# Kernel tuning notes

Hardware: AMD Instinct MI355X
Metric: run time of the kernel (lower is better)

Reference implementation:

```python
import jax, jax.numpy as jnp
import numpy as np

DIM, D_STATE, D_CONV, EXPAND = 1024, 16, 4, 2
D_INNER = EXPAND * DIM
DT_RANK = (DIM + 15) // 16  # 64
B, L = 2, 1024


def setup_inputs() -> dict:
    key = jax.random.key(0)
    ks = jax.random.split(key, 12)
    s = lambda k, shp, sc: jax.random.normal(k, shp, jnp.float32) * sc
    return {
        "x": s(ks[0], (B, L, DIM), 1.0),
        "ln_g": jnp.ones((DIM,), jnp.float32),
        "ln_b": jnp.zeros((DIM,), jnp.float32),
        "W_in": s(ks[1], (DIM, 2 * D_INNER), DIM ** -0.5),
        "conv_w": s(ks[2], (D_INNER, D_CONV), D_CONV ** -0.5),
        "conv_b": jnp.zeros((D_INNER,), jnp.float32),
        "W_x": s(ks[3], (D_INNER, DT_RANK + 2 * D_STATE), D_INNER ** -0.5),
        "W_dt": s(ks[4], (DT_RANK, D_INNER), DT_RANK ** -0.5),
        "b_dt": s(ks[5], (D_INNER,), 0.1),
        "A_log": jnp.log(jnp.broadcast_to(jnp.arange(1, D_STATE + 1, dtype=jnp.float32), (D_INNER, D_STATE))),
        "D_skip": jnp.ones((D_INNER,), jnp.float32),
        "W_out": s(ks[6], (D_INNER, DIM), D_INNER ** -0.5),
    }


def _mamba_block(x, ln_g, ln_b, W_in, conv_w, conv_b, W_x, W_dt, b_dt, A_log, D_skip, W_out):
    # LayerNorm over feature dim
    mu = jnp.mean(x, -1, keepdims=True)
    var = jnp.mean(jnp.square(x - mu), -1, keepdims=True)
    xn = (x - mu) * jax.lax.rsqrt(var + 1e-5) * ln_g + ln_b

    # in_proj -> (u, z), each (B, L, E)
    u, z = jnp.split(xn @ W_in, 2, axis=-1)

    # causal depthwise conv1d over L (kernel D_CONV) + SiLU
    up = jnp.pad(u, ((0, 0), (D_CONV - 1, 0), (0, 0)))
    uc = conv_b
    for k in range(D_CONV):
        uc = uc + conv_w[:, k] * up[:, k:k + L, :]
    uc = jax.nn.silu(uc)

    # input-dependent dt, B, C
    dbl = uc @ W_x
    dt = jax.nn.softplus(dbl[..., :DT_RANK] @ W_dt + b_dt)      # (B,L,E)
    Bc = dbl[..., DT_RANK:DT_RANK + D_STATE]                    # (B,L,N)
    Cc = dbl[..., DT_RANK + D_STATE:]                           # (B,L,N)

    A = -jnp.exp(A_log)                                         # (E,N)
    dA = jnp.exp(dt[..., None] * A)                             # (B,L,E,N)
    dBu = (dt * uc)[..., None] * Bc[:, :, None, :]              # (B,L,E,N)

    # selective scan: h_t = dA_t * h_{t-1} + dBu_t  (associative)
    def comb(c1, c2):
        a1, b1 = c1
        a2, b2 = c2
        return a2 * a1, a2 * b1 + b2

    _, h = jax.lax.associative_scan(comb, (dA, dBu), axis=1)

    y = jnp.einsum('blen,bln->ble', h, Cc) + uc * D_skip
    y = y * jax.nn.silu(z)
    return y @ W_out                                            # (B,L,DIM)


def reference(x, ln_g, ln_b, W_in, conv_w, conv_b, W_x, W_dt, b_dt, A_log, D_skip, W_out):
    return _mamba_block(x, ln_g, ln_b, W_in, conv_w, conv_b, W_x, W_dt, b_dt, A_log, D_skip, W_out)
```

## Files before the change

kernel.cpp:

```cpp
#include <hip/hip_runtime.h>
#include <hip/hip_bf16.h>

typedef __attribute__((ext_vector_type(4))) float  f32x4;
typedef __attribute__((ext_vector_type(8))) __bf16 bf16x8;
typedef __attribute__((ext_vector_type(8))) unsigned short u16x8;

typedef __attribute__((address_space(1))) void gvoid_t;
typedef __attribute__((address_space(3))) void lvoid_t;

__device__ __forceinline__ void gld16(const void* g, void* l) {
    __builtin_amdgcn_global_load_lds((const gvoid_t*)g, (lvoid_t*)l, 16, 0, 0);
}

template <int N> __device__ __forceinline__ void vwait() {
    if constexpr (N == 0)      asm volatile("s_waitcnt vmcnt(0)" ::: "memory");
    else if constexpr (N == 6) asm volatile("s_waitcnt vmcnt(6)" ::: "memory");
    else if constexpr (N == 8) asm volatile("s_waitcnt vmcnt(8)" ::: "memory");
}

__device__ __forceinline__ unsigned short f2bf(float f) {
    unsigned u = __builtin_bit_cast(unsigned, f);
    u += 0x7fffu + ((u >> 16) & 1u);
    return (unsigned short)(u >> 16);
}
__device__ __forceinline__ float bf2f(unsigned short u) {
    return __builtin_bit_cast(float, (unsigned)u << 16);
}
__device__ __forceinline__ float silu(float x) {
    return x / (1.f + __expf(-x));
}

__device__ __forceinline__ void powers16(float p, float* dA) {
    float p2 = p * p, p4 = p2 * p2, p8 = p4 * p4, p16 = p8 * p8;
    float q[5] = {p, p2, p4, p8, p16};
    #pragma unroll
    for (int n = 0; n < 16; ++n) {
        int m = n + 1;
        float r = 1.f;
        bool first = true;
        #pragma unroll
        for (int bit = 0; bit < 5; ++bit) {
            if (m & (1 << bit)) {
                r = first ? q[bit] : r * q[bit];
                first = false;
            }
        }
        dA[n] = r;
    }
}

__device__ __forceinline__ void tr_cvt(const float* __restrict__ in,
                                       unsigned short* __restrict__ out,
                                       int K, int N, int Npad, int bnb, int bkb,
                                       float* sh) {
    float (*t)[33] = (float(*)[33])sh;
    int bn = bnb * 32, bk = bkb * 32;
    int c = threadIdx.x & 31, r0 = threadIdx.x >> 5;
    #pragma unroll
    for (int rr = r0; rr < 32; rr += 8) {
        int k = bk + rr, n = bn + c;
        t[rr][c] = (k < K && n < N) ? in[(size_t)k * N + n] : 0.f;
    }
    __syncthreads();
    #pragma unroll
    for (int rr = r0; rr < 32; rr += 8) {
        int n = bn + rr, k = bk + c;
        if (n < Npad && k < K) out[(size_t)n * K + k] = f2bf(t[c][rr]);
    }
}

__global__ __launch_bounds__(256) void k_prep(const float* __restrict__ x,
                                              const float* __restrict__ g,
                                              const float* __restrict__ b,
                                              unsigned short* __restrict__ xn,
                                              const float* __restrict__ W_in,  unsigned short* __restrict__ WIN_T,
                                              const float* __restrict__ W_out, unsigned short* __restrict__ WOUT_T,
                                              const float* __restrict__ W_dt,  unsigned short* __restrict__ WDT_T,
                                              const float* __restrict__ W_x,   unsigned short* __restrict__ WX_T) {
    __shared__ float sh[32 * 33];
    int bid = blockIdx.x;
    if (bid < 2048) {
        int row = bid;
        const float4* xr = (const float4*)(x + (size_t)row * 1024);
        float4 v = xr[threadIdx.x];
        float s  = v.x + v.y + v.z + v.w;
        float ss = v.x*v.x + v.y*v.y + v.z*v.z + v.w*v.w;
        #pragma unroll
        for (int o = 32; o > 0; o >>= 1) { s += __shfl_down(s, o); ss += __shfl_down(ss, o); }
        if ((threadIdx.x & 63) == 0) { sh[threadIdx.x >> 6] = s; sh[4 + (threadIdx.x >> 6)] = ss; }
        __syncthreads();
        s  = sh[0] + sh[1] + sh[2] + sh[3];
        ss = sh[4] + sh[5] + sh[6] + sh[7];
        float mu  = s * (1.f / 1024.f);
        float inv = rsqrtf(ss * (1.f / 1024.f) - mu * mu + 1e-5f);
        float4 gv = ((const float4*)g)[threadIdx.x];
        float4 bv = ((const float4*)b)[threadIdx.x];
        ushort4 o4;
        o4.x = f2bf((v.x - mu) * inv * gv.x + bv.x);
        o4.y = f2bf((v.y - mu) * inv * gv.y + bv.y);
        o4.z = f2bf((v.z - mu) * inv * gv.z + bv.z);
        o4.w = f2bf((v.w - mu) * inv * gv.w + bv.w);
        ((ushort4*)xn)[(size_t)row * 256 + threadIdx.x] = o4;
    } else if (bid < 6144) {
        int i = bid - 2048;  tr_cvt(W_in,  WIN_T,  1024, 4096, 4096, i & 127, i >> 7, sh);
    } else if (bid < 8192) {
        int i = bid - 6144;  tr_cvt(W_out, WOUT_T, 2048, 1024, 1024, i & 31,  i >> 5, sh);
    } else if (bid < 8320) {
        int i = bid - 8192;  tr_cvt(W_dt,  WDT_T,  64,   2048, 2048, i & 63,  i >> 6, sh);
    } else {
        int i = bid - 8320;  tr_cvt(W_x,   WX_T,   2048, 96,   128,  i & 3,   i >> 2, sh);
    }
}

template <int BM, int BN, int EPI>
__global__ __launch_bounds__(256) void k_gemm2(const unsigned short* __restrict__ A,
                                               const unsigned short* __restrict__ Bt,
                                               float* __restrict__ C,
                                               unsigned short* __restrict__ C2,
                                               unsigned short* __restrict__ C3,
                                               int kchunk, int lda, int ldb, int ldc,
                                               size_t zstride,
                                               const float* __restrict__ bias) {
    constexpr int PA = BM / 32, PB = BN / 32, NV = PA + PB;
    constexpr int MF = BM / 32, NF = BN / 32;
    __shared__ __attribute__((aligned(16))) unsigned short sm[2 * BM * 64 + 2 * BN * 64];
    unsigned short* smA = sm;
    unsigned short* smB = sm + 2 * BM * 64;

    int tid = threadIdx.x, wave = tid >> 6, lane = tid & 63;
    int bm = blockIdx.x * BM, bn = blockIdx.y * BN;
    int kstart = blockIdx.z * kchunk;
    int nt = kchunk >> 6;
    C += (size_t)blockIdx.z * zstride;
    int wm = (wave >> 1) * (BM / 2), wn = (wave & 1) * (BN / 2);
    int lr = lane & 15, lq = lane >> 4;
    int srow = wave * 8 + (lane >> 3);
    int scg  = lane & 7;

    f32x4 acc[MF][NF] = {};

    auto STAGE = [&](int buf, int k0) {
        unsigned short* dA = smA + buf * (BM * 64) + wave * 512;
        unsigned short* dB = smB + buf * (BN * 64) + wave * 512;
        #pragma unroll
        for (int p = 0; p < PA; ++p) {
            int row = p * 32 + srow;
            int gcol = ((scg ^ (row & 7)) << 3) + k0;
            gld16(A + (size_t)(bm + row) * lda + gcol, dA + p * 2048);
        }
        #pragma unroll
        for (int p = 0; p < PB; ++p) {
            int row = p * 32 + srow;
            int gcol = ((scg ^ (row & 7)) << 3) + k0;
            gld16(Bt + (size_t)(bn + row) * ldb + gcol, dB + p * 2048);
        }
    };

    STAGE(0, kstart);
    for (int t = 0; t < nt; ++t) {
        int cur = t & 1;
        if (t + 1 < nt) { STAGE(cur ^ 1, kstart + (t + 1) * 64); vwait<NV>(); }
        else            { vwait<0>(); }
        __builtin_amdgcn_s_barrier();
        const unsigned short* sA = smA + cur * (BM * 64);
        const unsigned short* sB = smB + cur * (BN * 64);
        #pragma unroll
        for (int ks = 0; ks < 2; ++ks) {
            int cg = (ks * 4 + lq) ^ (lr & 7);
            bf16x8 af[MF], bfv[NF];
            #pragma unroll
            for (int i = 0; i < MF; ++i)
                af[i] = *(const bf16x8*)(sA + (wm + i * 16 + lr) * 64 + (cg << 3));
            #pragma unroll
            for (int i = 0; i < NF; ++i)
                bfv[i] = *(const bf16x8*)(sB + (wn + i * 16 + lr) * 64 + (cg << 3));
            #pragma unroll
            for (int mi = 0; mi < MF; ++mi)
                #pragma unroll
                for (int ni = 0; ni < NF; ++ni)
                    acc[mi][ni] = __builtin_amdgcn_mfma_f32_16x16x32_bf16(af[mi], bfv[ni], acc[mi][ni], 0, 0, 0);
        }
        __builtin_amdgcn_s_barrier();
    }

    if (EPI == 0) {
        constexpr int PADF = BN + 4;
        float* ftile = (float*)sm;
        #pragma unroll
        for (int mi = 0; mi < MF; ++mi)
            #pragma unroll
            for (int ni = 0; ni < NF; ++ni)
                #pragma unroll
                for (int v = 0; v < 4; ++v)
                    ftile[(wm + mi * 16 + (lq << 2) + v) * PADF + wn + ni * 16 + lr] = acc[mi][ni][v];
        __syncthreads();
        #pragma unroll
        for (int q = tid; q < BM * BN / 4; q += 256) {
            int row = q / (BN / 4);
            int cc  = (q % (BN / 4)) * 4;
            float4 vv = *(const float4*)(ftile + row * PADF + cc);
            *(float4*)(C + (size_t)(bm + row) * ldc + bn + cc) = vv;
        }
    } else {
        constexpr int PADH = BN + 8;
        unsigned short* stile = sm;
        unsigned short* dst;
        int bnn;
        if (EPI == 3) { dst = C2; bnn = bn; }
        else          { dst = (bn < 2048) ? C2 : C3; bnn = bn & 2047; }
        #pragma unroll
        for (int mi = 0; mi < MF; ++mi) {
            #pragma unroll
            for (int ni = 0; ni < NF; ++ni) {
                int c = bn + wn + ni * 16 + lr;
                #pragma unroll
                for (int v = 0; v < 4; ++v) {
                    float val = acc[mi][ni][v];
                    if (EPI == 3) {
                        val += bias[c];
                        val = (val > 20.f) ? val : log1pf(__expf(val));
                    } else if (bn >= 2048) {
                        val = silu(val);
                    }
                    stile[(wm + mi * 16 + (lq << 2) + v) * PADH + wn + ni * 16 + lr] = f2bf(val);
                }
            }
        }
        __syncthreads();
        #pragma unroll
        for (int q = tid; q < BM * BN / 8; q += 256) {
            int row = q / (BN / 8);
            int cc  = (q % (BN / 8)) * 8;
            u16x8 vv = *(const u16x8*)(stile + row * PADH + cc);
            *(u16x8*)(dst + (size_t)(bm + row) * ldc + bnn + cc) = vv;
        }
    }
}

__global__ __launch_bounds__(256) void k_red8(const float* __restrict__ part,
                                              float* __restrict__ dbl,
                                              unsigned short* __restrict__ dtr) {
    int idx = blockIdx.x * 256 + threadIdx.x;
    float s = 0.f;
    #pragma unroll
    for (int z = 0; z < 8; ++z) s += part[(size_t)z * 262144 + idx];
    dbl[idx] = s;
    int r = idx >> 7, c = idx & 127;
    if (c < 64) dtr[r * 64 + c] = f2bf(s);
}

__global__ __launch_bounds__(256) void k_conv2(const unsigned short* __restrict__ UB,
                                               const float* __restrict__ cw,
                                               const float* __restrict__ cb,
                                               unsigned short* __restrict__ ucb) {
    int idx = blockIdx.x * 256 + threadIdx.x;
    int e  = idx & 2047;
    int bl = idx >> 11;
    int l  = bl & 1023;
    float acc = cb[e];
    float4 wv = *(const float4*)(cw + e * 4);
    float w4[4] = {wv.x, wv.y, wv.z, wv.w};
    #pragma unroll
    for (int k = 0; k < 4; ++k) {
        int ls = l - 3 + k;
        if (ls >= 0) acc += w4[k] * bf2f(UB[(size_t)(bl - 3 + k) * 2048 + e]);
    }
    ucb[idx] = f2bf(silu(acc));
}


__global__ __launch_bounds__(256) void k_scan_p1(const unsigned short* __restrict__ ucb,
                                                 const unsigned short* __restrict__ dtb,
                                                 const float* __restrict__ dbl,
                                                 const float* __restrict__ A_log,
                                                 float* __restrict__ aggH,
                                                 float* __restrict__ sdtb) {
    __shared__ float sB[32][16];
    int bid = blockIdx.x;
    int c = bid & 31, eblk = (bid >> 5) & 7, b = bid >> 8;
    int t = threadIdx.x;
    int e = eblk * 256 + t;
    int bl0 = b * 1024 + c * 32;
    if (t < 128) {
        int r = t >> 2, j4 = t & 3;
        *(float4*)&sB[r][j4 * 4] = *(const float4*)(dbl + (size_t)(bl0 + r) * 128 + 64 + j4 * 4);
    }
    __syncthreads();
    float Aen[16];
    #pragma unroll
    for (int n = 0; n < 16; ++n) Aen[n] = -__expf(A_log[e * 16 + n]);
    bool fastA = true;
    #pragma unroll
    for (int n = 1; n < 16; ++n)
        fastA = fastA && (fabsf(Aen[n] - (n + 1) * Aen[0]) <= 1e-3f);
    float h[16];
    #pragma unroll
    for (int n = 0; n < 16; ++n) h[n] = 0.f;
    float sdt = 0.f;
    size_t iu = (size_t)bl0 * 2048 + e;
    #pragma unroll 4
    for (int l = 0; l < 32; ++l) {
        float dtv = bf2f(dtb[iu]);
        float ucv = bf2f(ucb[iu]);
        float dtu = dtv * ucv;
        float dA[16];
        if (fastA) powers16(__expf(dtv * Aen[0]), dA);
        else {
            #pragma unroll
            for (int n = 0; n < 16; ++n) dA[n] = __expf(dtv * Aen[n]);
        }
        #pragma unroll
        for (int n = 0; n < 16; ++n)
            h[n] = fmaf(dA[n], h[n], dtu * sB[l][n]);
        sdt += dtv;
        iu += 2048;
    }
    size_t o = ((size_t)(b * 32 + c) * 16) * 2048 + e;
    #pragma unroll
    for (int n = 0; n < 16; ++n) aggH[o + (size_t)n * 2048] = h[n];
    sdtb[(size_t)(b * 32 + c) * 2048 + e] = sdt;
}

__global__ __launch_bounds__(256) void k_scan_p2(const float* __restrict__ aggH,
                                                 const float* __restrict__ sdtb,
                                                 const float* __restrict__ A_log,
                                                 float* __restrict__ hinit) {
    int idx = blockIdx.x * 256 + threadIdx.x;
    int b = idx >> 15;
    int n = (idx >> 11) & 15;
    int e = idx & 2047;
    float Aen = -__expf(A_log[e * 16 + n]);
    float h = 0.f;
    #pragma unroll 4
    for (int c = 0; c < 32; ++c) {
        size_t base = ((size_t)(b * 32 + c) * 16 + n) * 2048 + e;
        hinit[base] = h;
        float a = __expf(sdtb[(size_t)(b * 32 + c) * 2048 + e] * Aen);
        h = fmaf(a, h, aggH[base]);
    }
}

__global__ __launch_bounds__(256) void k_scan_p3(const unsigned short* __restrict__ ucb,
                                                 const unsigned short* __restrict__ dtb,
                                                 const float* __restrict__ dbl,
                                                 const unsigned short* __restrict__ sz,
                                                 const float* __restrict__ A_log,
                                                 const float* __restrict__ D_skip,
                                                 const float* __restrict__ hinit,
                                                 unsigned short* __restrict__ yg) {
    __shared__ float sBC[32][32];
    int bid = blockIdx.x;
    int c = bid & 31, eblk = (bid >> 5) & 7, b = bid >> 8;
    int t = threadIdx.x;
    int e = eblk * 256 + t;
    int bl0 = b * 1024 + c * 32;
    {
        int r = t >> 3, j = t & 7;
        *(float4*)&sBC[r][j * 4] = *(const float4*)(dbl + (size_t)(bl0 + r) * 128 + 64 + j * 4);
    }
    __syncthreads();
    float Aen[16];
    #pragma unroll
    for (int n = 0; n < 16; ++n) Aen[n] = -__expf(A_log[e * 16 + n]);
    bool fastA = true;
    #pragma unroll
    for (int n = 1; n < 16; ++n)
        fastA = fastA && (fabsf(Aen[n] - (n + 1) * Aen[0]) <= 1e-3f);
    float De = D_skip[e];
    size_t o = ((size_t)(b * 32 + c) * 16) * 2048 + e;
    float h[16];
    #pragma unroll
    for (int n = 0; n < 16; ++n) h[n] = hinit[o + (size_t)n * 2048];
    size_t iu = (size_t)bl0 * 2048 + e;
    #pragma unroll 4
    for (int l = 0; l < 32; ++l) {
        float dtv = bf2f(dtb[iu]);
        float ucv = bf2f(ucb[iu]);
        float szv = bf2f(sz[iu]);
        float dtu = dtv * ucv;
        float dA[16];
        if (fastA) powers16(__expf(dtv * Aen[0]), dA);
        else {
            #pragma unroll
            for (int n = 0; n < 16; ++n) dA[n] = __expf(dtv * Aen[n]);
        }
        float y0 = 0.f, y1 = 0.f, y2 = 0.f, y3 = 0.f;
        #pragma unroll
        for (int n = 0; n < 16; n += 4) {
            h[n]     = fmaf(dA[n],     h[n],     dtu * sBC[l][n]);
            h[n + 1] = fmaf(dA[n + 1], h[n + 1], dtu * sBC[l][n + 1]);
            h[n + 2] = fmaf(dA[n + 2], h[n + 2], dtu * sBC[l][n + 2]);
            h[n + 3] = fmaf(dA[n + 3], h[n + 3], dtu * sBC[l][n + 3]);
            y0 = fmaf(h[n],     sBC[l][16 + n],     y0);
            y1 = fmaf(h[n + 1], sBC[l][16 + n + 1], y1);
            y2 = fmaf(h[n + 2], sBC[l][16 + n + 2], y2);
            y3 = fmaf(h[n + 3], sBC[l][16 + n + 3], y3);
        }
        float y = (y0 + y1) + (y2 + y3);
        y = (y + ucv * De) * szv;
        yg[iu] = f2bf(y);
        iu += 2048;
    }
}

extern "C" void kernel_launch(void* const* d_in, const int* in_sizes, int n_in,
                              void* d_out, int out_size, void* d_ws, size_t ws_size,
                              hipStream_t stream) {
    const float* x      = (const float*)d_in[0];
    const float* ln_g   = (const float*)d_in[1];
    const float* ln_b   = (const float*)d_in[2];
    const float* W_in   = (const float*)d_in[3];
    const float* conv_w = (const float*)d_in[4];
    const float* conv_b = (const float*)d_in[5];
    const float* W_x    = (const float*)d_in[6];
    const float* W_dt   = (const float*)d_in[7];
    const float* b_dt   = (const float*)d_in[8];
    const float* A_log  = (const float*)d_in[9];
    const float* D_skip = (const float*)d_in[10];
    const float* W_out  = (const float*)d_in[11];
    float* out = (float*)d_out;

    const size_t needed =
        (size_t)4096 * 1024 * 2 + (size_t)1024 * 2048 * 2 + (size_t)2048 * 64 * 2 +
        (size_t)128 * 2048 * 2 + (size_t)2048 * 1024 * 2 + (size_t)2048 * 4096 * 4 +
        (size_t)2048 * 2048 * 4 + (size_t)2048 * 2048 * 2 + (size_t)2048 * 128 * 4 +
        (size_t)2048 * 64 * 2 + (size_t)2048 * 2048 * 4 + (size_t)2048 * 2048 * 2;
    if (ws_size < needed) return;

    char* w = (char*)d_ws;
    unsigned short* WIN_T  = (unsigned short*)w; w += (size_t)4096 * 1024 * 2;
    unsigned short* WOUT_T = (unsigned short*)w; w += (size_t)1024 * 2048 * 2;
    unsigned short* WDT_T  = (unsigned short*)w; w += (size_t)2048 * 64 * 2;
    unsigned short* WX_T   = (unsigned short*)w; w += (size_t)128 * 2048 * 2;
    unsigned short* XN     = (unsigned short*)w; w += (size_t)2048 * 1024 * 2;
    unsigned short* UB     = (unsigned short*)w; w += (size_t)2048 * 2048 * 2;
    unsigned short* SZ     = (unsigned short*)w; w += (size_t)2048 * 2048 * 2;
    unsigned short* UCB    = (unsigned short*)w; w += (size_t)2048 * 2048 * 2;
    float*          DBL    = (float*)w;          w += (size_t)2048 * 128 * 4;
    unsigned short* DTR    = (unsigned short*)w; w += (size_t)2048 * 64 * 2;
    unsigned short* DTB    = (unsigned short*)w; w += (size_t)2048 * 2048 * 4;
    unsigned short* YG     = (unsigned short*)w; w += (size_t)2048 * 2048 * 2;

    float* PART  = (float*)WIN_T;
    float* AGGH  = (float*)WIN_T;
    float* SDT   = (float*)XN;
    float* HINIT = (float*)UB;

    k_prep<<<8576, 256, 0, stream>>>(x, ln_g, ln_b, XN,
                                     W_in, WIN_T, W_out, WOUT_T, W_dt, WDT_T, W_x, WX_T);

    k_gemm2<128, 128, 2><<<dim3(16, 32, 1), 256, 0, stream>>>(XN, WIN_T, nullptr, UB, SZ, 1024, 1024, 1024, 2048, 0, nullptr);

    k_conv2<<<16384, 256, 0, stream>>>(UB, conv_w, conv_b, UCB);

    k_gemm2<64, 128, 0><<<dim3(32, 1, 8), 256, 0, stream>>>(UCB, WX_T, PART, nullptr, nullptr, 256, 2048, 2048, 128, (size_t)2048 * 128, nullptr);

    k_red8<<<1024, 256, 0, stream>>>(PART, DBL, DTR);

    k_gemm2<128, 128, 3><<<dim3(16, 16, 1), 256, 0, stream>>>(DTR, WDT_T, nullptr, DTB, nullptr, 64, 64, 64, 2048, 0, b_dt);

    k_scan_p1<<<512, 256, 0, stream>>>(UCB, DTB, DBL, A_log, AGGH, SDT);
    k_scan_p2<<<256, 256, 0, stream>>>(AGGH, SDT, A_log, HINIT);
    k_scan_p3<<<512, 256, 0, stream>>>(UCB, DTB, DBL, SZ, A_log, D_skip, HINIT, YG);

    k_gemm2<64, 128, 0><<<dim3(32, 8, 1), 256, 0, stream>>>(YG, WOUT_T, out, nullptr, nullptr, 2048, 2048, 2048, 1024, 0, nullptr);
}
```

Measured before the change: 235.9 us.

## Swizzle in_proj GEMM blocks, vectorize conv, split scan into 64 chunks

```diff
diff --git a/kernel.cpp b/kernel.cpp
--- a/kernel.cpp
+++ b/kernel.cpp
@@ -112,7 +112,7 @@
     }
 }
 
-template <int BM, int BN, int EPI>
+template <int BM, int BN, int EPI, bool SWZ>
 __global__ __launch_bounds__(256) void k_gemm2(const unsigned short* __restrict__ A,
                                                const unsigned short* __restrict__ Bt,
                                                float* __restrict__ C,
@@ -128,7 +128,15 @@
     unsigned short* smB = sm + 2 * BM * 64;
 
     int tid = threadIdx.x, wave = tid >> 6, lane = tid & 63;
-    int bm = blockIdx.x * BM, bn = blockIdx.y * BN;
+    int bx = blockIdx.x, by = blockIdx.y;
+    if (SWZ) {
+        int gx  = gridDim.x;
+        int lin = bx + gx * by;
+        int cpx = (gx * gridDim.y) >> 3;
+        int nl  = (lin & 7) * cpx + (lin >> 3);
+        bx = nl % gx; by = nl / gx;
+    }
+    int bm = bx * BM, bn = by * BN;
     int kstart = blockIdx.z * kchunk;
     int nt = kchunk >> 6;
     C += (size_t)blockIdx.z * zstride;
@@ -254,18 +262,35 @@
                                                const float* __restrict__ cb,
                                                unsigned short* __restrict__ ucb) {
     int idx = blockIdx.x * 256 + threadIdx.x;
-    int e  = idx & 2047;
-    int bl = idx >> 11;
+    int e8 = idx & 255;
+    int bl = idx >> 8;
     int l  = bl & 1023;
-    float acc = cb[e];
-    float4 wv = *(const float4*)(cw + e * 4);
-    float w4[4] = {wv.x, wv.y, wv.z, wv.w};
+    int e  = e8 * 8;
+    float wv[8][4];
+    #pragma unroll
+    for (int j = 0; j < 8; ++j) {
+        float4 t = *(const float4*)(cw + (size_t)(e + j) * 4);
+        wv[j][0] = t.x; wv[j][1] = t.y; wv[j][2] = t.z; wv[j][3] = t.w;
+    }
+    float acc[8];
+    float4 cb0 = *(const float4*)(cb + e);
+    float4 cb1 = *(const float4*)(cb + e + 4);
+    acc[0] = cb0.x; acc[1] = cb0.y; acc[2] = cb0.z; acc[3] = cb0.w;
+    acc[4] = cb1.x; acc[5] = cb1.y; acc[6] = cb1.z; acc[7] = cb1.w;
     #pragma unroll
     for (int k = 0; k < 4; ++k) {
         int ls = l - 3 + k;
-        if (ls >= 0) acc += w4[k] * bf2f(UB[(size_t)(bl - 3 + k) * 2048 + e]);
-    }
-    ucb[idx] = f2bf(silu(acc));
+        if (ls >= 0) {
+            u16x8 uv = *(const u16x8*)(UB + (size_t)(bl - 3 + k) * 2048 + e);
+            #pragma unroll
+            for (int j = 0; j < 8; ++j)
+                acc[j] = fmaf(wv[j][k], bf2f(uv[j]), acc[j]);
+        }
+    }
+    u16x8 o;
+    #pragma unroll
+    for (int j = 0; j < 8; ++j) o[j] = f2bf(silu(acc[j]));
+    *(u16x8*)(ucb + (size_t)bl * 2048 + e) = o;
 }
 
 
@@ -275,13 +300,13 @@
                                                  const float* __restrict__ A_log,
                                                  float* __restrict__ aggH,
                                                  float* __restrict__ sdtb) {
-    __shared__ float sB[32][16];
+    __shared__ float sB[16][16];
     int bid = blockIdx.x;
-    int c = bid & 31, eblk = (bid >> 5) & 7, b = bid >> 8;
+    int c = bid & 63, eblk = (bid >> 6) & 7, b = bid >> 9;
     int t = threadIdx.x;
     int e = eblk * 256 + t;
-    int bl0 = b * 1024 + c * 32;
-    if (t < 128) {
+    int bl0 = b * 1024 + c * 16;
+    if (t < 64) {
         int r = t >> 2, j4 = t & 3;
         *(float4*)&sB[r][j4 * 4] = *(const float4*)(dbl + (size_t)(bl0 + r) * 128 + 64 + j4 * 4);
     }
@@ -299,7 +324,7 @@
     float sdt = 0.f;
     size_t iu = (size_t)bl0 * 2048 + e;
     #pragma unroll 4
-    for (int l = 0; l < 32; ++l) {
+    for (int l = 0; l < 16; ++l) {
         float dtv = bf2f(dtb[iu]);
         float ucv = bf2f(ucb[iu]);
         float dtu = dtv * ucv;
@@ -315,10 +340,10 @@
         sdt += dtv;
         iu += 2048;
     }
-    size_t o = ((size_t)(b * 32 + c) * 16) * 2048 + e;
+    size_t o = ((size_t)(b * 64 + c) * 16) * 2048 + e;
     #pragma unroll
     for (int n = 0; n < 16; ++n) aggH[o + (size_t)n * 2048] = h[n];
-    sdtb[(size_t)(b * 32 + c) * 2048 + e] = sdt;
+    sdtb[(size_t)(b * 64 + c) * 2048 + e] = sdt;
 }
 
 __global__ __launch_bounds__(256) void k_scan_p2(const float* __restrict__ aggH,
@@ -332,10 +357,10 @@
     float Aen = -__expf(A_log[e * 16 + n]);
     float h = 0.f;
     #pragma unroll 4
-    for (int c = 0; c < 32; ++c) {
-        size_t base = ((size_t)(b * 32 + c) * 16 + n) * 2048 + e;
+    for (int c = 0; c < 64; ++c) {
+        size_t base = ((size_t)(b * 64 + c) * 16 + n) * 2048 + e;
         hinit[base] = h;
-        float a = __expf(sdtb[(size_t)(b * 32 + c) * 2048 + e] * Aen);
+        float a = __expf(sdtb[(size_t)(b * 64 + c) * 2048 + e] * Aen);
         h = fmaf(a, h, aggH[base]);
     }
 }
@@ -348,13 +373,13 @@
                                                  const float* __restrict__ D_skip,
                                                  const float* __restrict__ hinit,
                                                  unsigned short* __restrict__ yg) {
-    __shared__ float sBC[32][32];
+    __shared__ float sBC[16][32];
     int bid = blockIdx.x;
-    int c = bid & 31, eblk = (bid >> 5) & 7, b = bid >> 8;
+    int c = bid & 63, eblk = (bid >> 6) & 7, b = bid >> 9;
     int t = threadIdx.x;
     int e = eblk * 256 + t;
-    int bl0 = b * 1024 + c * 32;
-    {
+    int bl0 = b * 1024 + c * 16;
+    if (t < 128) {
         int r = t >> 3, j = t & 7;
         *(float4*)&sBC[r][j * 4] = *(const float4*)(dbl + (size_t)(bl0 + r) * 128 + 64 + j * 4);
     }
@@ -367,13 +392,13 @@
     for (int n = 1; n < 16; ++n)
         fastA = fastA && (fabsf(Aen[n] - (n + 1) * Aen[0]) <= 1e-3f);
     float De = D_skip[e];
-    size_t o = ((size_t)(b * 32 + c) * 16) * 2048 + e;
+    size_t o = ((size_t)(b * 64 + c) * 16) * 2048 + e;
     float h[16];
     #pragma unroll
     for (int n = 0; n < 16; ++n) h[n] = hinit[o + (size_t)n * 2048];
     size_t iu = (size_t)bl0 * 2048 + e;
     #pragma unroll 4
-    for (int l = 0; l < 32; ++l) {
+    for (int l = 0; l < 16; ++l) {
         float dtv = bf2f(dtb[iu]);
         float ucv = bf2f(ucb[iu]);
         float szv = bf2f(sz[iu]);
@@ -424,7 +449,8 @@
         (size_t)4096 * 1024 * 2 + (size_t)1024 * 2048 * 2 + (size_t)2048 * 64 * 2 +
         (size_t)128 * 2048 * 2 + (size_t)2048 * 1024 * 2 + (size_t)2048 * 4096 * 4 +
         (size_t)2048 * 2048 * 4 + (size_t)2048 * 2048 * 2 + (size_t)2048 * 128 * 4 +
-        (size_t)2048 * 64 * 2 + (size_t)2048 * 2048 * 4 + (size_t)2048 * 2048 * 2;
+        (size_t)2048 * 64 * 2 + (size_t)2048 * 2048 * 4 + (size_t)2048 * 2048 * 2 +
+        (size_t)2 * 64 * 16 * 2048 * 4 * 2 + (size_t)2 * 64 * 2048 * 4;
     if (ws_size < needed) return;
 
     char* w = (char*)d_ws;
@@ -440,28 +466,28 @@
     unsigned short* DTR    = (unsigned short*)w; w += (size_t)2048 * 64 * 2;
     unsigned short* DTB    = (unsigned short*)w; w += (size_t)2048 * 2048 * 4;
     unsigned short* YG     = (unsigned short*)w; w += (size_t)2048 * 2048 * 2;
-
-    float* PART  = (float*)WIN_T;
-    float* AGGH  = (float*)WIN_T;
-    float* SDT   = (float*)XN;
-    float* HINIT = (float*)UB;
+    float*          AGGH   = (float*)w;          w += (size_t)2 * 64 * 16 * 2048 * 4;
+    float*          HINIT  = (float*)w;          w += (size_t)2 * 64 * 16 * 2048 * 4;
+    float*          SDT    = (float*)w;          w += (size_t)2 * 64 * 2048 * 4;
+
+    float* PART = (float*)WIN_T;
 
     k_prep<<<8576, 256, 0, stream>>>(x, ln_g, ln_b, XN,
                                      W_in, WIN_T, W_out, WOUT_T, W_dt, WDT_T, W_x, WX_T);
 
-    k_gemm2<128, 128, 2><<<dim3(16, 32, 1), 256, 0, stream>>>(XN, WIN_T, nullptr, UB, SZ, 1024, 1024, 1024, 2048, 0, nullptr);
-
-    k_conv2<<<16384, 256, 0, stream>>>(UB, conv_w, conv_b, UCB);
-
-    k_gemm2<64, 128, 0><<<dim3(32, 1, 8), 256, 0, stream>>>(UCB, WX_T, PART, nullptr, nullptr, 256, 2048, 2048, 128, (size_t)2048 * 128, nullptr);
+    k_gemm2<128, 128, 2, true><<<dim3(16, 32, 1), 256, 0, stream>>>(XN, WIN_T, nullptr, UB, SZ, 1024, 1024, 1024, 2048, 0, nullptr);
+
+    k_conv2<<<2048, 256, 0, stream>>>(UB, conv_w, conv_b, UCB);
+
+    k_gemm2<64, 128, 0, false><<<dim3(32, 1, 8), 256, 0, stream>>>(UCB, WX_T, PART, nullptr, nullptr, 256, 2048, 2048, 128, (size_t)2048 * 128, nullptr);
 
     k_red8<<<1024, 256, 0, stream>>>(PART, DBL, DTR);
 
-    k_gemm2<128, 128, 3><<<dim3(16, 16, 1), 256, 0, stream>>>(DTR, WDT_T, nullptr, DTB, nullptr, 64, 64, 64, 2048, 0, b_dt);
-
-    k_scan_p1<<<512, 256, 0, stream>>>(UCB, DTB, DBL, A_log, AGGH, SDT);
+    k_gemm2<128, 128, 3, false><<<dim3(16, 16, 1), 256, 0, stream>>>(DTR, WDT_T, nullptr, DTB, nullptr, 64, 64, 64, 2048, 0, b_dt);
+
+    k_scan_p1<<<1024, 256, 0, stream>>>(UCB, DTB, DBL, A_log, AGGH, SDT);
     k_scan_p2<<<256, 256, 0, stream>>>(AGGH, SDT, A_log, HINIT);
-    k_scan_p3<<<512, 256, 0, stream>>>(UCB, DTB, DBL, SZ, A_log, D_skip, HINIT, YG);
-
-    k_gemm2<64, 128, 0><<<dim3(32, 8, 1), 256, 0, stream>>>(YG, WOUT_T, out, nullptr, nullptr, 2048, 2048, 2048, 1024, 0, nullptr);
-}
+    k_scan_p3<<<1024, 256, 0, stream>>>(UCB, DTB, DBL, SZ, A_log, D_skip, HINIT, YG);
+
+    k_gemm2<64, 128, 0, false><<<dim3(32, 8, 1), 256, 0, stream>>>(YG, WOUT_T, out, nullptr, nullptr, 2048, 2048, 2048, 1024, 0, nullptr);
+}
```

Result: slower. 241.8 us (+2.5%).
